# Kernel optimization log

Measured on AMD Instinct MI355X. Metric: run time of the kernel, lower is better.

The kernel has to match this reference:

```python
import jax, jax.numpy as jnp
import numpy as np

K = 2  # Chebyshev order (filter_size)
OUT = 2  # output_size


def avwgcn(x, E, w_pool, b_pool):
    """Adaptive vertex-wise graph conv (AVWGCN).
    x: [B, N, C], E: [N, D], w_pool: [D, K, C, O], b_pool: [D, O]."""
    N = E.shape[0]
    # dynamic adjacency from node embeddings
    supports1 = jax.nn.softmax(jax.nn.relu(E @ E.T), axis=1)  # [N, N]
    s_set = [jnp.eye(N, dtype=x.dtype), supports1]
    for _ in range(2, K):
        s_set.append(2.0 * supports1 @ s_set[-1] - s_set[-2])
    supports = jnp.stack(s_set[:K])  # [K, N, N]
    W = jnp.einsum('nd,dkio->nkio', E, w_pool)  # per-node filters [N, K, C, O]
    b = E @ b_pool  # [N, O]
    x_g = jnp.einsum('knm,bmc->bnkc', supports, x)  # [B, N, K, C]
    return jnp.einsum('bnki,nkio->bno', x_g, W) + b


def setup_inputs() -> dict:
    key = jax.random.key(0)
    ks = jax.random.split(key, 8)
    B, N, C_IN, D = 16, 5570, 35, 4
    return {
        'x': jax.random.normal(ks[0], (B, N, C_IN), jnp.float32),
        'e': jax.random.normal(ks[1], (N, D), jnp.float32),
        'w_gate': jax.random.normal(ks[2], (D, K, C_IN + OUT, 2 * OUT), jnp.float32) * 0.1,
        'b_gate': jax.random.normal(ks[3], (D, 2 * OUT), jnp.float32) * 0.1,
        'w_update': jax.random.normal(ks[4], (D, K, C_IN + OUT, OUT), jnp.float32) * 0.1,
        'b_update': jax.random.normal(ks[5], (D, OUT), jnp.float32) * 0.1,
        'lin_w': jax.random.normal(ks[6], (OUT, 1), jnp.float32),
        'lin_b': jax.random.normal(ks[7], (1,), jnp.float32),
    }


def reference(x, e, w_gate, b_gate, w_update, b_update, lin_w, lin_b):
    B, N, _ = x.shape
    H = jnp.zeros((B, N, OUT), dtype=x.dtype)  # hidden state (None on first call)
    ZR = jax.nn.sigmoid(avwgcn(jnp.concatenate([x, H], axis=-1), e, w_gate, b_gate))
    Z, R = ZR[..., :OUT], ZR[..., OUT:]
    C = jnp.tanh(avwgcn(jnp.concatenate([x, Z * H], axis=-1), e, w_update, b_update))
    h0 = R * H + (1.0 - R) * C  # [B, N, OUT]
    y = jax.nn.relu(h0) @ lin_w + lin_b  # [B, N, 1]
    return y
```

## Files before the change

kernel.cpp:

```cpp
#include <hip/hip_runtime.h>
#include <hip/hip_bf16.h>
#include <math.h>

#define NN   5570
#define BB   16
#define CIN  35
#define MPAD 5632
#define NCHUNK 176
#define OUTER 11
#define CPS  16

#define OFF_RSUM 0
#define OFF_G0C  61952
#define OFF_PGP  418432
#define OFF_GTF  4339712

typedef __attribute__((ext_vector_type(8))) short  short8;
typedef __attribute__((ext_vector_type(4))) float  floatx4;

static __device__ inline ushort f2bf(float f) {
    union { __hip_bfloat16 h; ushort u; } cv;
    cv.h = __float2bfloat16(f);
    return cv.u;
}

__global__ __launch_bounds__(256)
void kg_g(const float* __restrict__ x, const float* __restrict__ e,
          const float* __restrict__ wg, const float* __restrict__ wu,
          float* __restrict__ g0c, ushort* __restrict__ gtf) {
    __shared__ float xs[256 * CIN];
    __shared__ float wl[8 * CIN * 4];
    __shared__ ushort ls[256 * 17];
    int tid = threadIdx.x;
    int b   = blockIdx.y;
    int m0  = blockIdx.x * 256;

    for (int i = tid; i < 8 * CIN * 4; i += 256) {
        int j = i & 3, rest = i >> 2;
        int c = rest % CIN, kd = rest / CIN;
        int k = kd >> 2, d = kd & 3;
        float v;
        if (j < 2) v = wg[((d * 2 + k) * 37 + c) * 4 + 2 + j];
        else       v = wu[((d * 2 + k) * 37 + c) * 2 + (j - 2)];
        wl[i] = v;
    }
    int rows = NN - m0; if (rows > 256) rows = 256; if (rows < 0) rows = 0;
    const float* xsrc = x + ((size_t)b * NN + m0) * CIN;
    for (int i = tid; i < rows * CIN; i += 256) xs[i] = xsrc[i];
    __syncthreads();

    int m = m0 + tid;
    float a1[16];
    #pragma unroll
    for (int i = 0; i < 16; ++i) a1[i] = 0.f;

    if (m < NN) {
        float a0[16];
        #pragma unroll
        for (int i = 0; i < 16; ++i) a0[i] = 0.f;
        for (int c = 0; c < CIN; ++c) {
            float xa = xs[tid * CIN + c];
            #pragma unroll
            for (int kd = 0; kd < 8; ++kd) {
                const float4 w = *(const float4*)&wl[(kd * CIN + c) * 4];
                const int d4 = (kd & 3) * 4;
                if (kd < 4) {
                    a0[d4+0] += xa*w.x; a0[d4+1] += xa*w.y;
                    a0[d4+2] += xa*w.z; a0[d4+3] += xa*w.w;
                } else {
                    a1[d4+0] += xa*w.x; a1[d4+1] += xa*w.y;
                    a1[d4+2] += xa*w.z; a1[d4+3] += xa*w.w;
                }
            }
        }
        float4 em4 = ((const float4*)e)[m];
        float p0[4];
        #pragma unroll
        for (int j = 0; j < 4; ++j)
            p0[j] = em4.x*a0[j] + em4.y*a0[4+j] + em4.z*a0[8+j] + em4.w*a0[12+j];
        ((float4*)g0c)[(size_t)b * NN + m] = make_float4(p0[0], p0[1], p0[2], p0[3]);
    }

    #pragma unroll
    for (int dj = 0; dj < 16; ++dj) ls[tid * 17 + dj] = f2bf(a1[dj]);
    __syncthreads();

    const int wave = tid >> 6, lane = tid & 63;
    const int qo = lane >> 4, dj = lane & 15;
    #pragma unroll
    for (int i = 0; i < 2; ++i) {
        const int lc = wave * 2 + i;
        const int ck = blockIdx.x * 8 + lc;
        short8 v;
        #pragma unroll
        for (int u = 0; u < 8; ++u)
            v[u] = (short)ls[(lc * 32 + qo * 8 + u) * 17 + dj];
        *(short8*)&gtf[((size_t)(ck * 16 + b)) * 512 + lane * 8] = v;
    }
}

static __device__ inline void load_chunk(const ushort* __restrict__ gsrc,
                                         ushort* ldst, int tid, int wave) {
    #pragma unroll
    for (int i = 0; i < 4; ++i) {
        const ushort* g = gsrc + (size_t)(i * 256 + tid) * 8;
        ushort* l = ldst + (size_t)(i * 256 + wave * 64) * 8;
        __builtin_amdgcn_global_load_lds(
            (const __attribute__((address_space(1))) unsigned int*)g,
            (__attribute__((address_space(3))) unsigned int*)l, 16, 0, 0);
    }
}

template <bool CHECK>
__device__ __forceinline__ void kb_main(const float4* __restrict__ esl,
                                        const ushort* __restrict__ gsl,
                                        ushort (*sbuf)[8192],
                                        const float4 en, int k0m,
                                        int tid, int wave, int lane, int quad,
                                        floatx4 (&acc)[16], float& rowsum) {
    #pragma unroll 2
    for (int st = 0; st < CPS; ++st) {
        __syncthreads();
        if (st + 1 < CPS)
            load_chunk(gsl + (size_t)(st + 1) * 8192, sbuf[(st + 1) & 1], tid, wave);

        short8 af;
        const int stq = st * 32 + quad * 8;
        const int ux  = (st * 4 + quad) & 7;
        #pragma unroll
        for (int u = 0; u < 8; ++u) {
            float4 em = esl[stq + (u ^ ux)];
            float dt = en.x*em.x + en.y*em.y + en.z*em.z + en.w*em.w;
            float sv = __expf(fmaxf(dt, 0.f));
            if (CHECK && (k0m + stq + u >= NN)) sv = 0.f;
            rowsum += sv;
            af[u] = (short)f2bf(sv);
        }

        const ushort* bb = &sbuf[st & 1][lane * 8];
        #pragma unroll
        for (int ct = 0; ct < 16; ++ct) {
            short8 bf = *(const short8*)&bb[ct * 512];
            acc[ct] = __builtin_amdgcn_mfma_f32_16x16x32_bf16(af, bf, acc[ct], 0, 0, 0);
        }
    }
}

__global__ __launch_bounds__(256, 4)
void kb_pg(const float* __restrict__ e, const ushort* __restrict__ gtf,
           float* __restrict__ pgp, float* __restrict__ rsums) {
    __shared__ ushort sbuf[2][8192];
    __shared__ float4 esl[512];
    const int tid  = threadIdx.x;
    const int wave = tid >> 6;
    const int lane = tid & 63;
    const int l15  = lane & 15;
    const int quad = lane >> 4;
    const int rt   = blockIdx.x * 4 + wave;
    const int s    = blockIdx.y;
    const int k0m  = s * (CPS * 32);
    const float4* E4 = (const float4*)e;

    for (int i = tid; i < 512; i += 256) {
        int m = k0m + i;
        esl[i ^ ((i >> 3) & 7)] = (m < NN) ? E4[m] : make_float4(0.f, 0.f, 0.f, 0.f);
    }
    const ushort* gsl = gtf + (size_t)s * CPS * 8192;
    load_chunk(gsl, sbuf[0], tid, wave);

    const int nr = rt * 16 + l15;
    const float4 en = E4[nr < NN ? nr : 0];

    floatx4 acc[16];
    #pragma unroll
    for (int i = 0; i < 16; ++i) acc[i] = (floatx4){0.f, 0.f, 0.f, 0.f};
    float rowsum = 0.f;

    if (k0m + CPS * 32 <= NN)
        kb_main<false>(esl, gsl, sbuf, en, k0m, tid, wave, lane, quad, acc, rowsum);
    else
        kb_main<true >(esl, gsl, sbuf, en, k0m, tid, wave, lane, quad, acc, rowsum);

    rowsum += __shfl_xor(rowsum, 16);
    rowsum += __shfl_xor(rowsum, 32);
    if (quad == 0) rsums[(size_t)s * MPAD + nr] = rowsum;

    const int dsel = l15 >> 2, jj = l15 & 3;
    float end[4];
    #pragma unroll
    for (int j = 0; j < 4; ++j) {
        int n = rt * 16 + quad * 4 + j;
        end[j] = (n < NN) ? e[n * 4 + dsel] : 0.f;
    }
    #pragma unroll
    for (int ct = 0; ct < 16; ++ct) {
        #pragma unroll
        for (int j = 0; j < 4; ++j) {
            float v = end[j] * acc[ct][j];
            v += __shfl_xor(v, 4);
            v += __shfl_xor(v, 8);
            int n = rt * 16 + quad * 4 + j;
            if (l15 < 4 && n < NN)
                pgp[(((size_t)s * BB + ct) * NN + n) * 4 + jj] = v;
        }
    }
}

static __device__ inline float fsig(float x) {
    return 1.f / (1.f + __expf(-x));
}
static __device__ inline float ftanh(float x) {
    float t = __expf(fminf(2.f * x, 80.f));
    return (t - 1.f) / (t + 1.f);
}

__global__ __launch_bounds__(256)
void ke_out(const float* __restrict__ e, const float* __restrict__ rsums,
            const float* __restrict__ g0c, const float* __restrict__ pgp,
            const float* __restrict__ bg, const float* __restrict__ bu,
            const float* __restrict__ lw, const float* __restrict__ lb,
            float* __restrict__ out) {
    int n = blockIdx.x * 256 + threadIdx.x;
    int b = blockIdx.y;
    if (n >= NN) return;
    float4 ev = ((const float4*)e)[n];
    float ed[4] = {ev.x, ev.y, ev.z, ev.w};
    float den = 0.f;
    #pragma unroll
    for (int s = 0; s < OUTER; ++s) den += rsums[(size_t)s * MPAD + n];
    float rd = 1.f / den;

    float pgf[4] = {0.f, 0.f, 0.f, 0.f};
    #pragma unroll
    for (int s = 0; s < OUTER; ++s) {
        float4 t = ((const float4*)pgp)[((size_t)s * BB + b) * NN + n];
        pgf[0] += t.x; pgf[1] += t.y; pgf[2] += t.z; pgf[3] += t.w;
    }
    float4 g0v = ((const float4*)g0c)[(size_t)b * NN + n];
    float g0f[4] = {g0v.x, g0v.y, g0v.z, g0v.w};

    float pre[4];
    #pragma unroll
    for (int j = 0; j < 4; ++j) {
        float bj = 0.f;
        #pragma unroll
        for (int d = 0; d < 4; ++d) {
            float bp = (j < 2) ? bg[d * 4 + 2 + j] : bu[d * 2 + (j - 2)];
            bj += ed[d] * bp;
        }
        pre[j] = g0f[j] + rd * pgf[j] + bj;
    }
    float R0 = fsig(pre[0]);
    float R1 = fsig(pre[1]);
    float C0 = ftanh(pre[2]);
    float C1 = ftanh(pre[3]);
    float h0 = (1.f - R0) * C0;
    float h1 = (1.f - R1) * C1;
    float y = fmaxf(h0, 0.f) * lw[0] + fmaxf(h1, 0.f) * lw[1] + lb[0];
    out[(size_t)b * NN + n] = y;
}

extern "C" void kernel_launch(void* const* d_in, const int* in_sizes, int n_in,
                              void* d_out, int out_size, void* d_ws, size_t ws_size,
                              hipStream_t stream) {
    const float* x  = (const float*)d_in[0];
    const float* e  = (const float*)d_in[1];
    const float* wg = (const float*)d_in[2];
    const float* bg = (const float*)d_in[3];
    const float* wu = (const float*)d_in[4];
    const float* bu = (const float*)d_in[5];
    const float* lw = (const float*)d_in[6];
    const float* lb = (const float*)d_in[7];
    float* out = (float*)d_out;

    float*  wsf   = (float*)d_ws;
    float*  rsums = wsf + OFF_RSUM;
    float*  g0c   = wsf + OFF_G0C;
    float*  pgp   = wsf + OFF_PGP;
    ushort* gtf   = (ushort*)(wsf + OFF_GTF);

    hipLaunchKernelGGL(kg_g, dim3(22, 16), dim3(256), 0, stream, x, e, wg, wu, g0c, gtf);
    hipLaunchKernelGGL(kb_pg, dim3(88, OUTER), dim3(256), 0, stream, e, gtf, pgp, rsums);
    hipLaunchKernelGGL(ke_out, dim3(22, 16), dim3(256), 0, stream,
                       e, rsums, g0c, pgp, bg, bu, lw, lb, out);
}
```

Baseline: 124.7 us.

## Give each wave two row tiles in kb_pg to reuse shared-memory B fragments

Each wave in kb_pg now computes two 16-row tiles instead of one, so each B fragment read from shared memory feeds two MFMAs. Blocks shrink from four waves to two while covering the same 64 rows, which halves LDS reads of B and the number of block barriers per row. The cost is double the accumulator registers (32 floatx4 per lane), which may cut occupancy (launch bounds now 128 threads, min 2 blocks). Fewer threads also issue the global-to-LDS copies, so each thread does twice as many loads.

New measurement: 131.5 us. +5.5%, slower.

```diff
diff --git a/kernel.cpp b/kernel.cpp
--- a/kernel.cpp
+++ b/kernel.cpp
@@ -102,9 +102,9 @@
 static __device__ inline void load_chunk(const ushort* __restrict__ gsrc,
                                          ushort* ldst, int tid, int wave) {
     #pragma unroll
-    for (int i = 0; i < 4; ++i) {
-        const ushort* g = gsrc + (size_t)(i * 256 + tid) * 8;
-        ushort* l = ldst + (size_t)(i * 256 + wave * 64) * 8;
+    for (int i = 0; i < 8; ++i) {
+        const ushort* g = gsrc + (size_t)(i * 128 + tid) * 8;
+        ushort* l = ldst + (size_t)(i * 128 + wave * 64) * 8;
         __builtin_amdgcn_global_load_lds(
             (const __attribute__((address_space(1))) unsigned int*)g,
             (__attribute__((address_space(3))) unsigned int*)l, 16, 0, 0);
@@ -115,38 +115,43 @@
 __device__ __forceinline__ void kb_main(const float4* __restrict__ esl,
                                         const ushort* __restrict__ gsl,
                                         ushort (*sbuf)[8192],
-                                        const float4 en, int k0m,
-                                        int tid, int wave, int lane, int quad,
-                                        floatx4 (&acc)[16], float& rowsum) {
+                                        const float4 en0, const float4 en1,
+                                        int k0m, int tid, int wave, int lane,
+                                        int quad, floatx4 (&acc)[2][16],
+                                        float& rowsum0, float& rowsum1) {
     #pragma unroll 2
     for (int st = 0; st < CPS; ++st) {
         __syncthreads();
         if (st + 1 < CPS)
             load_chunk(gsl + (size_t)(st + 1) * 8192, sbuf[(st + 1) & 1], tid, wave);
 
-        short8 af;
+        short8 af0, af1;
         const int stq = st * 32 + quad * 8;
         const int ux  = (st * 4 + quad) & 7;
         #pragma unroll
         for (int u = 0; u < 8; ++u) {
             float4 em = esl[stq + (u ^ ux)];
-            float dt = en.x*em.x + en.y*em.y + en.z*em.z + en.w*em.w;
-            float sv = __expf(fmaxf(dt, 0.f));
-            if (CHECK && (k0m + stq + u >= NN)) sv = 0.f;
-            rowsum += sv;
-            af[u] = (short)f2bf(sv);
+            float d0 = en0.x*em.x + en0.y*em.y + en0.z*em.z + en0.w*em.w;
+            float d1 = en1.x*em.x + en1.y*em.y + en1.z*em.z + en1.w*em.w;
+            float s0 = __expf(fmaxf(d0, 0.f));
+            float s1 = __expf(fmaxf(d1, 0.f));
+            if (CHECK && (k0m + stq + u >= NN)) { s0 = 0.f; s1 = 0.f; }
+            rowsum0 += s0; rowsum1 += s1;
+            af0[u] = (short)f2bf(s0);
+            af1[u] = (short)f2bf(s1);
         }
 
         const ushort* bb = &sbuf[st & 1][lane * 8];
         #pragma unroll
         for (int ct = 0; ct < 16; ++ct) {
             short8 bf = *(const short8*)&bb[ct * 512];
-            acc[ct] = __builtin_amdgcn_mfma_f32_16x16x32_bf16(af, bf, acc[ct], 0, 0, 0);
-        }
-    }
-}
-
-__global__ __launch_bounds__(256, 4)
+            acc[0][ct] = __builtin_amdgcn_mfma_f32_16x16x32_bf16(af0, bf, acc[0][ct], 0, 0, 0);
+            acc[1][ct] = __builtin_amdgcn_mfma_f32_16x16x32_bf16(af1, bf, acc[1][ct], 0, 0, 0);
+        }
+    }
+}
+
+__global__ __launch_bounds__(128, 2)
 void kb_pg(const float* __restrict__ e, const ushort* __restrict__ gtf,
            float* __restrict__ pgp, float* __restrict__ rsums) {
     __shared__ ushort sbuf[2][8192];
@@ -156,52 +161,66 @@
     const int lane = tid & 63;
     const int l15  = lane & 15;
     const int quad = lane >> 4;
-    const int rt   = blockIdx.x * 4 + wave;
+    const int wr0  = (blockIdx.x * 2 + wave) * 32;
     const int s    = blockIdx.y;
     const int k0m  = s * (CPS * 32);
     const float4* E4 = (const float4*)e;
 
-    for (int i = tid; i < 512; i += 256) {
+    for (int i = tid; i < 512; i += 128) {
         int m = k0m + i;
         esl[i ^ ((i >> 3) & 7)] = (m < NN) ? E4[m] : make_float4(0.f, 0.f, 0.f, 0.f);
     }
     const ushort* gsl = gtf + (size_t)s * CPS * 8192;
     load_chunk(gsl, sbuf[0], tid, wave);
 
-    const int nr = rt * 16 + l15;
-    const float4 en = E4[nr < NN ? nr : 0];
-
-    floatx4 acc[16];
-    #pragma unroll
-    for (int i = 0; i < 16; ++i) acc[i] = (floatx4){0.f, 0.f, 0.f, 0.f};
-    float rowsum = 0.f;
+    const int nr0 = wr0 + l15, nr1 = wr0 + 16 + l15;
+    const float4 en0 = E4[nr0 < NN ? nr0 : 0];
+    const float4 en1 = E4[nr1 < NN ? nr1 : 0];
+
+    floatx4 acc[2][16];
+    #pragma unroll
+    for (int t = 0; t < 2; ++t)
+        #pragma unroll
+        for (int i = 0; i < 16; ++i) acc[t][i] = (floatx4){0.f, 0.f, 0.f, 0.f};
+    float rowsum0 = 0.f, rowsum1 = 0.f;
 
     if (k0m + CPS * 32 <= NN)
-        kb_main<false>(esl, gsl, sbuf, en, k0m, tid, wave, lane, quad, acc, rowsum);
+        kb_main<false>(esl, gsl, sbuf, en0, en1, k0m, tid, wave, lane, quad,
+                       acc, rowsum0, rowsum1);
     else
-        kb_main<true >(esl, gsl, sbuf, en, k0m, tid, wave, lane, quad, acc, rowsum);
-
-    rowsum += __shfl_xor(rowsum, 16);
-    rowsum += __shfl_xor(rowsum, 32);
-    if (quad == 0) rsums[(size_t)s * MPAD + nr] = rowsum;
+        kb_main<true >(esl, gsl, sbuf, en0, en1, k0m, tid, wave, lane, quad,
+                       acc, rowsum0, rowsum1);
+
+    rowsum0 += __shfl_xor(rowsum0, 16);
+    rowsum0 += __shfl_xor(rowsum0, 32);
+    rowsum1 += __shfl_xor(rowsum1, 16);
+    rowsum1 += __shfl_xor(rowsum1, 32);
+    if (quad == 0) {
+        rsums[(size_t)s * MPAD + nr0] = rowsum0;
+        rsums[(size_t)s * MPAD + nr1] = rowsum1;
+    }
 
     const int dsel = l15 >> 2, jj = l15 & 3;
-    float end[4];
-    #pragma unroll
-    for (int j = 0; j < 4; ++j) {
-        int n = rt * 16 + quad * 4 + j;
-        end[j] = (n < NN) ? e[n * 4 + dsel] : 0.f;
-    }
-    #pragma unroll
-    for (int ct = 0; ct < 16; ++ct) {
+    #pragma unroll
+    for (int t = 0; t < 2; ++t) {
+        const int nbase = wr0 + t * 16;
+        float end[4];
         #pragma unroll
         for (int j = 0; j < 4; ++j) {
-            float v = end[j] * acc[ct][j];
-            v += __shfl_xor(v, 4);
-            v += __shfl_xor(v, 8);
-            int n = rt * 16 + quad * 4 + j;
-            if (l15 < 4 && n < NN)
-                pgp[(((size_t)s * BB + ct) * NN + n) * 4 + jj] = v;
+            int n = nbase + quad * 4 + j;
+            end[j] = (n < NN) ? e[n * 4 + dsel] : 0.f;
+        }
+        #pragma unroll
+        for (int ct = 0; ct < 16; ++ct) {
+            #pragma unroll
+            for (int j = 0; j < 4; ++j) {
+                float v = end[j] * acc[t][ct][j];
+                v += __shfl_xor(v, 4);
+                v += __shfl_xor(v, 8);
+                int n = nbase + quad * 4 + j;
+                if (l15 < 4 && n < NN)
+                    pgp[(((size_t)s * BB + ct) * NN + n) * 4 + jj] = v;
+            }
         }
     }
 }
@@ -280,7 +299,7 @@
     ushort* gtf   = (ushort*)(wsf + OFF_GTF);
 
     hipLaunchKernelGGL(kg_g, dim3(22, 16), dim3(256), 0, stream, x, e, wg, wu, g0c, gtf);
-    hipLaunchKernelGGL(kb_pg, dim3(88, OUTER), dim3(256), 0, stream, e, gtf, pgp, rsums);
+    hipLaunchKernelGGL(kb_pg, dim3(88, OUTER), dim3(128), 0, stream, e, gtf, pgp, rsums);
     hipLaunchKernelGGL(ke_out, dim3(22, 16), dim3(256), 0, stream,
                        e, rsums, g0c, pgp, bg, bu, lw, lb, out);
 }
```
